# Kernel tuning notes

Measured on AMD Instinct MI355X. Metric: run time of the kernel, lower is better.

The kernel has to match this reference:

```python
import jax, jax.numpy as jnp
import numpy as np

N_NODES = 50000
N_EDGES = 1600000
IN_FEATS = 256
OUT_FEATS = 64


def setup_inputs() -> dict:
    key = jax.random.key(0)
    k1, k2, k3, k4, k5, k6 = jax.random.split(key, 6)
    feature = jax.random.normal(k1, (N_NODES, IN_FEATS), dtype=jnp.float32)
    src = jax.random.randint(k2, (N_EDGES,), 0, N_NODES, dtype=jnp.int32)
    dst = jax.random.randint(k3, (N_EDGES,), 0, N_NODES, dtype=jnp.int32)
    # parameters (xavier-ish scaling)
    W = jax.random.normal(k4, (OUT_FEATS, IN_FEATS), dtype=jnp.float32) * np.sqrt(2.0 / (IN_FEATS + OUT_FEATS))
    att_w = jax.random.normal(k5, (1, 2 * OUT_FEATS), dtype=jnp.float32) * np.sqrt(2.0 / (2 * OUT_FEATS + 1))
    bias = jax.random.normal(k6, (1, OUT_FEATS), dtype=jnp.float32) * np.sqrt(2.0 / (1 + OUT_FEATS))
    return {"feature": feature, "W": W, "att_w": att_w, "bias": bias, "src": src, "dst": dst}


def reference(feature, W, att_w, bias, src, dst):
    # Wh = linear(feature)   [N, out]
    Wh = feature @ W.T
    # concat([Wh_src, Wh_dst]) @ att_w.T  ==  Wh_src@a_src + Wh_dst@a_dst
    a_src = att_w[0, :OUT_FEATS]
    a_dst = att_w[0, OUT_FEATS:]
    el = Wh @ a_src  # [N]
    er = Wh @ a_dst  # [N]
    e = el[src] + er[dst]  # [E]
    e = jax.nn.leaky_relu(e, negative_slope=0.2)
    # segment softmax over incoming edges of each dst node
    e_max = jax.ops.segment_max(e, dst, num_segments=N_NODES)  # -inf for empty
    e_max = jnp.where(jnp.isfinite(e_max), e_max, 0.0)
    e_exp = jnp.exp(e - e_max[dst])
    denom = jax.ops.segment_sum(e_exp, dst, num_segments=N_NODES)
    alpha = e_exp / jnp.where(denom[dst] > 0, denom[dst], 1.0)  # [E]
    # scatter-weighted sum of source features
    h_new = jax.ops.segment_sum(alpha[:, None] * Wh[src], dst, num_segments=N_NODES)
    # residual + bias + activation
    h_new = h_new + Wh
    h_new = jax.nn.elu(h_new + bias)
    return h_new
```

## Files before the change

### kernel.cpp

```cpp
#include <hip/hip_runtime.h>
#include <hip/hip_bf16.h>
#include <math.h>

#define N_NODES 50000
#define N_EDGES 1600000
#define IN_F 256
#define OUT_F 64

#define NBUCKETS 391
#define CAP 4736
#define GEMM_BLOCKS 782
#define BK_BLOCKS 782
#define EPB 2048

typedef short short8 __attribute__((ext_vector_type(8)));
typedef float f32x4 __attribute__((ext_vector_type(4)));

__device__ __forceinline__ unsigned short f2bf(float f) {
    union { __hip_bfloat16 h; unsigned short u; } v;
    v.h = __float2bfloat16(f);
    return v.u;
}
__device__ __forceinline__ float bf2f(unsigned u) {
    return __uint_as_float(u << 16);
}

__global__ __launch_bounds__(256) void k_prep(const float* __restrict__ W,
                                              unsigned short* __restrict__ wfrag,
                                              int* __restrict__ cnt) {
    const int tid = threadIdx.x;
    if (blockIdx.x == 0)
        for (int i = tid; i < NBUCKETS; i += 256) cnt[i] = 0;
    int c = blockIdx.x * 256 + tid;
    int ct = c >> 9, kt = (c >> 6) & 7, cl = c & 63;
    int col = ct * 16 + (cl & 15);
    int kb = kt * 32 + 8 * (cl >> 4);
    const float* p = W + col * 256 + kb;
    float4 x = *(const float4*)p;
    float4 y = *(const float4*)(p + 4);
    short8 v;
    v[0] = f2bf(x.x); v[1] = f2bf(x.y); v[2] = f2bf(x.z); v[3] = f2bf(x.w);
    v[4] = f2bf(y.x); v[5] = f2bf(y.y); v[6] = f2bf(y.z); v[7] = f2bf(y.w);
    *(short8*)(wfrag + c * 8) = v;
}

__global__ __launch_bounds__(256) void k_main(const float* __restrict__ feat,
                                              const unsigned short* __restrict__ wfrag,
                                              const float* __restrict__ att_w,
                                              unsigned short* __restrict__ whb,
                                              float* __restrict__ el,
                                              float* __restrict__ er,
                                              const int* __restrict__ src,
                                              const int* __restrict__ dst,
                                              int* __restrict__ cnt,
                                              unsigned* __restrict__ pairs) {
    const int tid = threadIdx.x;

    if (blockIdx.x >= GEMM_BLOCKS) {
        __shared__ int lhist[NBUCKETS];
        __shared__ int lcur[NBUCKETS];
        const int beg = (blockIdx.x - GEMM_BLOCKS) * EPB;
        int end = beg + EPB; if (end > N_EDGES) end = N_EDGES;
        for (int i = tid; i < NBUCKETS; i += 256) lhist[i] = 0;
        __syncthreads();

        int e0 = beg + tid * 8;
        int n = (e0 < end) ? ((end - e0 < 8) ? (end - e0) : 8) : 0;
        int d[8], s[8];
        if (n == 8) {
            int4 a = *(const int4*)(dst + e0), b = *(const int4*)(dst + e0 + 4);
            int4 c = *(const int4*)(src + e0), q = *(const int4*)(src + e0 + 4);
            d[0]=a.x; d[1]=a.y; d[2]=a.z; d[3]=a.w; d[4]=b.x; d[5]=b.y; d[6]=b.z; d[7]=b.w;
            s[0]=c.x; s[1]=c.y; s[2]=c.z; s[3]=c.w; s[4]=q.x; s[5]=q.y; s[6]=q.z; s[7]=q.w;
        } else {
            #pragma unroll
            for (int j = 0; j < 8; ++j) { d[j] = (j < n) ? dst[e0 + j] : 0; s[j] = (j < n) ? src[e0 + j] : 0; }
        }
        #pragma unroll
        for (int j = 0; j < 8; ++j) if (j < n) atomicAdd(&lhist[d[j] >> 7], 1);
        __syncthreads();
        for (int i = tid; i < NBUCKETS; i += 256) {
            int c = lhist[i];
            lcur[i] = c ? (i * CAP + atomicAdd(&cnt[i], c)) : 0;
        }
        __syncthreads();
        #pragma unroll
        for (int j = 0; j < 8; ++j) if (j < n) {
            int pos = atomicAdd(&lcur[d[j] >> 7], 1);
            pairs[pos] = (unsigned)s[j] | ((unsigned)(d[j] & 127) << 16);
        }
        return;
    }

    const int l = tid & 63, w = tid >> 6;
    const int l15 = l & 15, lg = l >> 4;
    const int wbase = blockIdx.x * 64 + w * 16;
    int ar = wbase + l15; if (ar > N_NODES - 1) ar = N_NODES - 1;
    const float* fbase = feat + (size_t)ar * IN_F + 8 * lg;
    const unsigned short* wfl = wfrag + l * 8;

    f32x4 acc[4];
    #pragma unroll
    for (int ct = 0; ct < 4; ++ct) acc[ct] = (f32x4){0.f, 0.f, 0.f, 0.f};

    float4 fa = *(const float4*)(fbase);
    float4 fb = *(const float4*)(fbase + 4);
    #pragma unroll
    for (int kt = 0; kt < 8; ++kt) {
        float4 na, nb;
        if (kt < 7) {
            na = *(const float4*)(fbase + (kt + 1) * 32);
            nb = *(const float4*)(fbase + (kt + 1) * 32 + 4);
        }
        short8 bf0 = *(const short8*)(wfl + (0 * 8 + kt) * 512);
        short8 bf1 = *(const short8*)(wfl + (1 * 8 + kt) * 512);
        short8 bf2 = *(const short8*)(wfl + (2 * 8 + kt) * 512);
        short8 bf3 = *(const short8*)(wfl + (3 * 8 + kt) * 512);
        short8 af;
        af[0] = f2bf(fa.x); af[1] = f2bf(fa.y); af[2] = f2bf(fa.z); af[3] = f2bf(fa.w);
        af[4] = f2bf(fb.x); af[5] = f2bf(fb.y); af[6] = f2bf(fb.z); af[7] = f2bf(fb.w);
        acc[0] = __builtin_amdgcn_mfma_f32_16x16x32_bf16(af, bf0, acc[0], 0, 0, 0);
        acc[1] = __builtin_amdgcn_mfma_f32_16x16x32_bf16(af, bf1, acc[1], 0, 0, 0);
        acc[2] = __builtin_amdgcn_mfma_f32_16x16x32_bf16(af, bf2, acc[2], 0, 0, 0);
        acc[3] = __builtin_amdgcn_mfma_f32_16x16x32_bf16(af, bf3, acc[3], 0, 0, 0);
        fa = na; fb = nb;
    }

    float asrc[4], adst[4];
    #pragma unroll
    for (int ct = 0; ct < 4; ++ct) {
        asrc[ct] = att_w[ct * 16 + l15];
        adst[ct] = att_w[64 + ct * 16 + l15];
    }
    #pragma unroll
    for (int j = 0; j < 4; ++j) {
        int row = wbase + lg * 4 + j;
        float vs = 0.f, vd = 0.f;
        #pragma unroll
        for (int ct = 0; ct < 4; ++ct) {
            float v = acc[ct][j];
            vs += v * asrc[ct];
            vd += v * adst[ct];
            if (row < N_NODES) whb[(size_t)row * OUT_F + ct * 16 + l15] = f2bf(v);
        }
        vs += __shfl_xor(vs, 1); vd += __shfl_xor(vd, 1);
        vs += __shfl_xor(vs, 2); vd += __shfl_xor(vd, 2);
        vs += __shfl_xor(vs, 4); vd += __shfl_xor(vd, 4);
        vs += __shfl_xor(vs, 8); vd += __shfl_xor(vd, 8);
        if (l15 == 0 && row < N_NODES) { el[row] = vs; er[row] = vd; }
    }
}

__global__ __launch_bounds__(1024) void k_build(const int* __restrict__ cnt,
                                                const unsigned* __restrict__ pairs,
                                                const float* __restrict__ el,
                                                const float* __restrict__ er,
                                                int* __restrict__ offs,
                                                int* __restrict__ oend,
                                                unsigned* __restrict__ csr) {
    __shared__ int lcnt[128], ssc[128], lcur[128];
    __shared__ float ler[128];
    const int b = blockIdx.x;
    const int t = threadIdx.x;
    const int ebeg = b * CAP;
    const int nE = cnt[b];

    if (t < 128) {
        lcnt[t] = 0;
        int node = b * 128 + t;
        ler[t] = (node < N_NODES) ? er[node] : 0.f;
    }
    __syncthreads();
    for (int i = t; i < nE; i += 1024)
        atomicAdd(&lcnt[(pairs[ebeg + i] >> 16) & 127], 1);
    __syncthreads();
    if (t < 128) ssc[t] = lcnt[t];
    __syncthreads();
    for (int d = 1; d < 128; d <<= 1) {
        int v = 0;
        if (t < 128 && t >= d) v = ssc[t - d];
        __syncthreads();
        if (t < 128) ssc[t] += v;
        __syncthreads();
    }
    if (t < 128) {
        int base = ssc[t] - lcnt[t];
        lcur[t] = base;
        int node = b * 128 + t;
        if (node < N_NODES) { offs[node] = ebeg + base; oend[node] = ebeg + base + lcnt[t]; }
    }
    __syncthreads();
    for (int i = t; i < nE; i += 1024) {
        unsigned v = pairs[ebeg + i];
        int n7 = (v >> 16) & 127;
        int s = v & 0xFFFFu;
        float e = el[s] + ler[n7];
        e = (e > 0.f) ? e : 0.2f * e;
        float p = __expf(e);
        int pos = atomicAdd(&lcur[n7], 1);
        csr[ebeg + pos] = (unsigned)s | ((unsigned)f2bf(p) << 16);
    }
}

__global__ __launch_bounds__(256) void k_aggr(const int* __restrict__ offs,
                                              const int* __restrict__ oend,
                                              const unsigned* __restrict__ csr,
                                              const unsigned short* __restrict__ whb,
                                              const float* __restrict__ bias,
                                              float* __restrict__ out) {
    const int wid = __builtin_amdgcn_readfirstlane(threadIdx.x >> 6);
    const int node = blockIdx.x * 4 + wid;
    const int lane = threadIdx.x & 63;
    const int beg = offs[node], end = oend[node];

    float acc = 0.f, den = 0.f;
    #pragma unroll 4
    for (int j = beg; j < end; ++j) {
        unsigned e = csr[j];
        float p = bf2f(e >> 16);
        unsigned short wv = whb[(size_t)(e & 0xFFFFu) * OUT_F + lane];
        acc = fmaf(p, bf2f((unsigned)wv), acc);
        den += p;
    }
    float inv = (end > beg) ? 1.f / den : 0.f;
    float h = acc * inv + bf2f((unsigned)whb[(size_t)node * OUT_F + lane]) + bias[lane];
    out[(size_t)node * OUT_F + lane] = (h > 0.f) ? h : __expf(h) - 1.f;
}

extern "C" void kernel_launch(void* const* d_in, const int* in_sizes, int n_in,
                              void* d_out, int out_size, void* d_ws, size_t ws_size,
                              hipStream_t stream) {
    const float* feat  = (const float*)d_in[0];
    const float* W     = (const float*)d_in[1];
    const float* att_w = (const float*)d_in[2];
    const float* bias  = (const float*)d_in[3];
    const int*   src   = (const int*)d_in[4];
    const int*   dst   = (const int*)d_in[5];
    float* out = (float*)d_out;

    unsigned short* whb = (unsigned short*)d_ws;
    unsigned short* wfrag = whb + 3200000;
    float* el      = (float*)d_ws + 1600000 + 8192;
    float* er      = el + 50048;
    int*   offs    = (int*)(er + 50048);
    int*   oend    = offs + 50048;
    int*   cnt     = oend + 50048;
    unsigned* pairs = (unsigned*)(cnt + 512);
    unsigned* csr   = pairs + NBUCKETS * CAP;

    k_prep<<<8, 256, 0, stream>>>(W, wfrag, cnt);
    k_main<<<GEMM_BLOCKS + BK_BLOCKS, 256, 0, stream>>>(feat, wfrag, att_w, whb, el, er,
                                                        src, dst, cnt, pairs);
    k_build<<<NBUCKETS, 1024, 0, stream>>>(cnt, pairs, el, er, offs, oend, csr);
    k_aggr<<<N_NODES / 4, 256, 0, stream>>>(offs, oend, csr, whb, bias, out);
}
```

Measured before the change: 95.51 us.

## Process four edges per wave in aggregation with padded CSR and wider buckets

The aggregation kernel now splits each wavefront into four 16-lane groups. Each group handles a different edge and loads four bf16 features per lane, and the partial sums are combined with cross-lane shuffles. To support this, the CSR build pads each node's edge list to a multiple of four with zero entries. Buckets are widened to 256 nodes, with fewer, larger binning blocks and a simpler strided binning loop. The intent is more memory-level parallelism and fewer loop iterations in the gather-bound aggregation, at the cost of padding writes, shuffle reductions, and larger per-bucket capacity.

After: 91.87 us. 3.8% less time.

```diff
diff --git a/kernel.cpp b/kernel.cpp
--- a/kernel.cpp
+++ b/kernel.cpp
@@ -7,11 +7,11 @@
 #define IN_F 256
 #define OUT_F 64
 
-#define NBUCKETS 391
-#define CAP 4736
+#define NBUCKETS 196
+#define CAP 10240
 #define GEMM_BLOCKS 782
-#define BK_BLOCKS 782
-#define EPB 2048
+#define BK_BLOCKS 391
+#define EPB 4096
 
 typedef short short8 __attribute__((ext_vector_type(8)));
 typedef float f32x4 __attribute__((ext_vector_type(4)));
@@ -29,8 +29,7 @@
                                               unsigned short* __restrict__ wfrag,
                                               int* __restrict__ cnt) {
     const int tid = threadIdx.x;
-    if (blockIdx.x == 0)
-        for (int i = tid; i < NBUCKETS; i += 256) cnt[i] = 0;
+    if (blockIdx.x == 0 && tid < NBUCKETS) cnt[tid] = 0;
     int c = blockIdx.x * 256 + tid;
     int ct = c >> 9, kt = (c >> 6) & 7, cl = c & 63;
     int col = ct * 16 + (cl & 15);
@@ -61,33 +60,20 @@
         __shared__ int lcur[NBUCKETS];
         const int beg = (blockIdx.x - GEMM_BLOCKS) * EPB;
         int end = beg + EPB; if (end > N_EDGES) end = N_EDGES;
-        for (int i = tid; i < NBUCKETS; i += 256) lhist[i] = 0;
-        __syncthreads();
-
-        int e0 = beg + tid * 8;
-        int n = (e0 < end) ? ((end - e0 < 8) ? (end - e0) : 8) : 0;
-        int d[8], s[8];
-        if (n == 8) {
-            int4 a = *(const int4*)(dst + e0), b = *(const int4*)(dst + e0 + 4);
-            int4 c = *(const int4*)(src + e0), q = *(const int4*)(src + e0 + 4);
-            d[0]=a.x; d[1]=a.y; d[2]=a.z; d[3]=a.w; d[4]=b.x; d[5]=b.y; d[6]=b.z; d[7]=b.w;
-            s[0]=c.x; s[1]=c.y; s[2]=c.z; s[3]=c.w; s[4]=q.x; s[5]=q.y; s[6]=q.z; s[7]=q.w;
-        } else {
-            #pragma unroll
-            for (int j = 0; j < 8; ++j) { d[j] = (j < n) ? dst[e0 + j] : 0; s[j] = (j < n) ? src[e0 + j] : 0; }
-        }
-        #pragma unroll
-        for (int j = 0; j < 8; ++j) if (j < n) atomicAdd(&lhist[d[j] >> 7], 1);
-        __syncthreads();
-        for (int i = tid; i < NBUCKETS; i += 256) {
-            int c = lhist[i];
-            lcur[i] = c ? (i * CAP + atomicAdd(&cnt[i], c)) : 0;
-        }
-        __syncthreads();
-        #pragma unroll
-        for (int j = 0; j < 8; ++j) if (j < n) {
-            int pos = atomicAdd(&lcur[d[j] >> 7], 1);
-            pairs[pos] = (unsigned)s[j] | ((unsigned)(d[j] & 127) << 16);
+        if (tid < NBUCKETS) lhist[tid] = 0;
+        __syncthreads();
+        for (int i = beg + tid; i < end; i += 256)
+            atomicAdd(&lhist[dst[i] >> 8], 1);
+        __syncthreads();
+        if (tid < NBUCKETS) {
+            int c = lhist[tid];
+            lcur[tid] = c ? (tid * CAP + atomicAdd(&cnt[tid], c)) : 0;
+        }
+        __syncthreads();
+        for (int i = beg + tid; i < end; i += 256) {
+            int d = dst[i];
+            int pos = atomicAdd(&lcur[d >> 8], 1);
+            pairs[pos] = (unsigned)src[i] | ((unsigned)(d & 255) << 16);
         }
         return;
     }
@@ -158,46 +144,48 @@
                                                 int* __restrict__ offs,
                                                 int* __restrict__ oend,
                                                 unsigned* __restrict__ csr) {
-    __shared__ int lcnt[128], ssc[128], lcur[128];
-    __shared__ float ler[128];
+    __shared__ int lcnt[256], ssc[256], lcur[256];
+    __shared__ float ler[256];
     const int b = blockIdx.x;
     const int t = threadIdx.x;
     const int ebeg = b * CAP;
     const int nE = cnt[b];
 
-    if (t < 128) {
+    if (t < 256) {
         lcnt[t] = 0;
-        int node = b * 128 + t;
+        int node = b * 256 + t;
         ler[t] = (node < N_NODES) ? er[node] : 0.f;
     }
     __syncthreads();
     for (int i = t; i < nE; i += 1024)
-        atomicAdd(&lcnt[(pairs[ebeg + i] >> 16) & 127], 1);
-    __syncthreads();
-    if (t < 128) ssc[t] = lcnt[t];
-    __syncthreads();
-    for (int d = 1; d < 128; d <<= 1) {
+        atomicAdd(&lcnt[(pairs[ebeg + i] >> 16) & 255], 1);
+    __syncthreads();
+    if (t < 256) ssc[t] = (lcnt[t] + 3) & ~3;
+    __syncthreads();
+    for (int d = 1; d < 256; d <<= 1) {
         int v = 0;
-        if (t < 128 && t >= d) v = ssc[t - d];
-        __syncthreads();
-        if (t < 128) ssc[t] += v;
-        __syncthreads();
-    }
-    if (t < 128) {
-        int base = ssc[t] - lcnt[t];
+        if (t < 256 && t >= d) v = ssc[t - d];
+        __syncthreads();
+        if (t < 256) ssc[t] += v;
+        __syncthreads();
+    }
+    if (t < 256) {
+        int pc = (lcnt[t] + 3) & ~3;
+        int base = ssc[t] - pc;
         lcur[t] = base;
-        int node = b * 128 + t;
-        if (node < N_NODES) { offs[node] = ebeg + base; oend[node] = ebeg + base + lcnt[t]; }
+        int node = b * 256 + t;
+        if (node < N_NODES) { offs[node] = ebeg + base; oend[node] = ebeg + base + pc; }
+        for (int k = lcnt[t]; k < pc; ++k) csr[ebeg + base + k] = 0;
     }
     __syncthreads();
     for (int i = t; i < nE; i += 1024) {
         unsigned v = pairs[ebeg + i];
-        int n7 = (v >> 16) & 127;
+        int n8 = (v >> 16) & 255;
         int s = v & 0xFFFFu;
-        float e = el[s] + ler[n7];
+        float e = el[s] + ler[n8];
         e = (e > 0.f) ? e : 0.2f * e;
         float p = __expf(e);
-        int pos = atomicAdd(&lcur[n7], 1);
+        int pos = atomicAdd(&lcur[n8], 1);
         csr[ebeg + pos] = (unsigned)s | ((unsigned)f2bf(p) << 16);
     }
 }
@@ -211,20 +199,42 @@
     const int wid = __builtin_amdgcn_readfirstlane(threadIdx.x >> 6);
     const int node = blockIdx.x * 4 + wid;
     const int lane = threadIdx.x & 63;
+    const int fg = lane & 15, es = lane >> 4;
     const int beg = offs[node], end = oend[node];
 
-    float acc = 0.f, den = 0.f;
-    #pragma unroll 4
-    for (int j = beg; j < end; ++j) {
-        unsigned e = csr[j];
-        float p = bf2f(e >> 16);
-        unsigned short wv = whb[(size_t)(e & 0xFFFFu) * OUT_F + lane];
-        acc = fmaf(p, bf2f((unsigned)wv), acc);
+    float acc0 = 0.f, acc1 = 0.f, acc2 = 0.f, acc3 = 0.f, den = 0.f;
+    #pragma unroll 2
+    for (int j = beg; j < end; j += 4) {
+        unsigned e = csr[j + es];
+        float p = __uint_as_float(e & 0xFFFF0000u);
+        const unsigned short* wp = whb + (size_t)(e & 0xFFFFu) * OUT_F + fg * 4;
+        ushort4 wv = *(const ushort4*)wp;
         den += p;
-    }
-    float inv = (end > beg) ? 1.f / den : 0.f;
-    float h = acc * inv + bf2f((unsigned)whb[(size_t)node * OUT_F + lane]) + bias[lane];
-    out[(size_t)node * OUT_F + lane] = (h > 0.f) ? h : __expf(h) - 1.f;
+        acc0 = fmaf(p, bf2f((unsigned)wv.x), acc0);
+        acc1 = fmaf(p, bf2f((unsigned)wv.y), acc1);
+        acc2 = fmaf(p, bf2f((unsigned)wv.z), acc2);
+        acc3 = fmaf(p, bf2f((unsigned)wv.w), acc3);
+    }
+    acc0 += __shfl_xor(acc0, 16); acc0 += __shfl_xor(acc0, 32);
+    acc1 += __shfl_xor(acc1, 16); acc1 += __shfl_xor(acc1, 32);
+    acc2 += __shfl_xor(acc2, 16); acc2 += __shfl_xor(acc2, 32);
+    acc3 += __shfl_xor(acc3, 16); acc3 += __shfl_xor(acc3, 32);
+    den  += __shfl_xor(den, 16);  den  += __shfl_xor(den, 32);
+
+    if (es == 0) {
+        float inv = (end > beg) ? 1.f / den : 0.f;
+        ushort4 wn = *(const ushort4*)(whb + (size_t)node * OUT_F + fg * 4);
+        float4 b4 = *(const float4*)(bias + fg * 4);
+        float h0 = acc0 * inv + bf2f((unsigned)wn.x) + b4.x;
+        float h1 = acc1 * inv + bf2f((unsigned)wn.y) + b4.y;
+        float h2 = acc2 * inv + bf2f((unsigned)wn.z) + b4.z;
+        float h3 = acc3 * inv + bf2f((unsigned)wn.w) + b4.w;
+        h0 = (h0 > 0.f) ? h0 : __expf(h0) - 1.f;
+        h1 = (h1 > 0.f) ? h1 : __expf(h1) - 1.f;
+        h2 = (h2 > 0.f) ? h2 : __expf(h2) - 1.f;
+        h3 = (h3 > 0.f) ? h3 : __expf(h3) - 1.f;
+        *(float4*)(out + (size_t)node * OUT_F + fg * 4) = make_float4(h0, h1, h2, h3);
+    }
 }
 
 extern "C" void kernel_launch(void* const* d_in, const int* in_sizes, int n_in,
```
